# Kernel tuning notes

Hardware: AMD Instinct MI355X
Metric: run time of the kernel (lower is better)

Reference implementation:

```python
import jax, jax.numpy as jnp
import numpy as np

B, L, E, H = 4, 4096, 1024, 16
HD = E // H
I = 4096  # intermediate_size = 4*E
RMS_EPS = 1e-6
ATTN_EPS = 1e-6
GATE_INIT = 0.1  # 0.1 + 0.05*layer_idx, layer_idx=0


def rmsnorm(x, w, eps=RMS_EPS):
    xf = x.astype(jnp.float32)
    var = jnp.mean(xf * xf, axis=-1, keepdims=True)
    return w * (xf * jax.lax.rsqrt(var + eps)).astype(x.dtype)


def rotate_half(x):
    d = x.shape[-1] // 2
    return jnp.concatenate([-x[..., d:], x[..., :d]], axis=-1)


def setup_inputs() -> dict:
    key = jax.random.key(0)
    ks = jax.random.split(key, 16)
    h = jax.random.normal(ks[0], (B, L, E), jnp.float32)
    c = jax.random.normal(ks[1], (B, E), jnp.float32)
    # standard RoPE tables, shape (L, HD)
    pos = jnp.arange(L, dtype=jnp.float32)
    inv = 1.0 / (10000.0 ** (jnp.arange(0, HD, 2, dtype=jnp.float32) / HD))
    fr = pos[:, None] * inv[None, :]
    emb = jnp.concatenate([fr, fr], axis=-1)
    cos, sin = jnp.cos(emb), jnp.sin(emb)
    s = 0.02
    Wq = jax.random.normal(ks[2], (E, E), jnp.float32) * s
    Wk = jax.random.normal(ks[3], (E, E), jnp.float32) * s
    Wv = jax.random.normal(ks[4], (E, E), jnp.float32) * s
    Wo = jax.random.normal(ks[5], (E, E), jnp.float32) * s
    Wg = jax.random.normal(ks[6], (I, E), jnp.float32) * s
    Wu = jax.random.normal(ks[7], (I, E), jnp.float32) * s
    Wd = jax.random.normal(ks[8], (E, I), jnp.float32) * s
    w_norm1 = jnp.ones((E,), jnp.float32)
    w_norm2 = jnp.ones((E,), jnp.float32)
    Wada = jax.random.normal(ks[9], (6 * E, E), jnp.float32) * 0.01
    bada = np.zeros((6 * E,), np.float32)
    bada[2 * E:3 * E] = GATE_INIT  # gate_msa
    bada[5 * E:6 * E] = GATE_INIT  # gate_mlp
    bada = jnp.asarray(bada)
    return {"h": h, "c": c, "cos": cos, "sin": sin, "Wq": Wq, "Wk": Wk,
            "Wv": Wv, "Wo": Wo, "Wg": Wg, "Wu": Wu, "Wd": Wd,
            "w_norm1": w_norm1, "w_norm2": w_norm2, "Wada": Wada, "bada": bada}


def reference(h, c, cos, sin, Wq, Wk, Wv, Wo, Wg, Wu, Wd, w_norm1, w_norm2, Wada, bada):
    # adaLN modulation: (B, 6E) -> six (B,1,E) chunks
    mod = c @ Wada.T + bada
    sh1, sc1, g1, sh2, sc2, g2 = [m[:, None, :] for m in jnp.split(mod, 6, axis=-1)]

    # --- attention branch ---
    x = rmsnorm(h, w_norm1) * (1.0 + sc1) + sh1  # modulate
    q = jax.nn.silu(x @ Wq.T).reshape(B, L, H, HD).transpose(0, 2, 1, 3)  # (B,H,L,hd)
    k = jax.nn.silu(x @ Wk.T).reshape(B, L, H, HD).transpose(0, 2, 1, 3)
    v = (x @ Wv.T).reshape(B, L, H, HD).transpose(0, 2, 1, 3)
    cs = cos[None, None]  # (1,1,L,hd)
    sn = sin[None, None]
    q = q * cs + rotate_half(q) * sn
    k = k * cs + rotate_half(k) * sn
    # cosFormer sin/cos feature map; m = max(src,tgt) = L
    idx = (np.pi / 2) * jnp.arange(1, L + 1, dtype=jnp.float32) / L  # (L,)
    sw = jnp.sin(idx)[None, None, :, None]
    cw = jnp.cos(idx)[None, None, :, None]
    q_ = jnp.concatenate([q * sw, q * cw], axis=-1)  # (B,H,L,2hd)
    k_ = jnp.concatenate([k * sw, k * cw], axis=-1)
    # non-causal linear attention: K^T V first (O(L))
    kv = jnp.einsum('bhld,bhlm->bhdm', k_, v)             # (B,H,2hd,hd)
    z = 1.0 / jnp.maximum(jnp.einsum('bhld,bhd->bhl', q_, k_.sum(axis=2)), ATTN_EPS)
    attn = jnp.einsum('bhld,bhdm,bhl->bhlm', q_, kv, z)   # (B,H,L,hd)
    attn = attn.transpose(0, 2, 1, 3).reshape(B, L, E) @ Wo.T
    h = h + g1 * attn  # bias_dropout_add_scale, eval mode

    # --- MLP branch ---
    x = rmsnorm(h, w_norm2) * (1.0 + sc2) + sh2
    mlp = (jax.nn.silu(x @ Wg.T) * (x @ Wu.T)) @ Wd.T
    return h + g2 * mlp
```

## Files before the change

### kernel.cpp

```cpp
#include <hip/hip_runtime.h>
#include <hip/hip_bf16.h>

#define BB 4
#define LL 4096
#define EE 1024
#define HH 16
#define II 4096
#define MM (BB*LL)

using f32x4 = __attribute__((ext_vector_type(4))) float;
using s16x8 = __attribute__((ext_vector_type(8))) short;
using u32x4 = __attribute__((ext_vector_type(4))) unsigned int;

__device__ __forceinline__ unsigned short f2bf(float f) {
  union { float f; unsigned u; } x; x.f = f;
  unsigned r = x.u + 0x7fffu + ((x.u >> 16) & 1u);
  return (unsigned short)(r >> 16);
}
__device__ __forceinline__ float bf2f(unsigned short s) {
  union { unsigned u; float f; } x; x.u = ((unsigned)s) << 16;
  return x.f;
}
__device__ __forceinline__ float silu_f(float x) { return x / (1.0f + expf(-x)); }

__device__ __forceinline__ void gll16(const void* g, void* l) {
  __builtin_amdgcn_global_load_lds(
      (const __attribute__((address_space(1))) unsigned int*)g,
      (__attribute__((address_space(3))) unsigned int*)l, 16, 0, 0);
}

__global__ __launch_bounds__(256) void k_mod(const float* __restrict__ c,
    const float* __restrict__ Wada, const float* __restrict__ bada,
    float* __restrict__ mod) {
  __shared__ float cs[EE];
  int b = blockIdx.y;
  int n = blockIdx.x * 256 + threadIdx.x;
  for (int i = threadIdx.x; i < EE; i += 256) cs[i] = c[b*EE + i];
  __syncthreads();
  const float4* wp = (const float4*)(Wada + (size_t)n * EE);
  float acc = 0.f;
  for (int k = 0; k < EE/4; k++) {
    float4 t = wp[k];
    acc += t.x*cs[4*k] + t.y*cs[4*k+1] + t.z*cs[4*k+2] + t.w*cs[4*k+3];
  }
  mod[(size_t)b*6*EE + n] = acc + bada[n];
}

__global__ __launch_bounds__(256) void k_coef(const float* __restrict__ mod,
    const float* __restrict__ w1, const float* __restrict__ w2,
    float* __restrict__ cf1, float* __restrict__ cf2) {
  int k = blockIdx.x * 256 + threadIdx.x;
  int b = blockIdx.y;
  const float* mb = mod + (size_t)b*6*EE;
  cf1[(size_t)b*2048 + k]        = w1[k] * (1.0f + mb[EE + k]);
  cf1[(size_t)b*2048 + 1024 + k] = mb[k];
  cf2[(size_t)b*2048 + k]        = w2[k] * (1.0f + mb[4*EE + k]);
  cf2[(size_t)b*2048 + 1024 + k] = mb[3*EE + k];
}

__global__ __launch_bounds__(256) void k_rsig(const float* __restrict__ in,
    float* __restrict__ rsig) {
  int row = blockIdx.x;
  int t = threadIdx.x;
  float4 v = ((const float4*)(in + (size_t)row * EE))[t];
  float ss = v.x*v.x + v.y*v.y + v.z*v.z + v.w*v.w;
  #pragma unroll
  for (int o = 32; o > 0; o >>= 1) ss += __shfl_down(ss, o, 64);
  __shared__ float red[4];
  if ((t & 63) == 0) red[t >> 6] = ss;
  __syncthreads();
  float tot = red[0] + red[1] + red[2] + red[3];
  if (t == 0) rsig[row] = 1.0f / sqrtf(tot * (1.0f/1024.0f) + 1e-6f);
}

__global__ __launch_bounds__(256) void k_f2b(const float* __restrict__ s,
    unsigned short* __restrict__ d, int n4) {
  int i = blockIdx.x * 256 + threadIdx.x;
  if (i >= n4) return;
  float4 v = ((const float4*)s)[i];
  ushort4 u; u.x = f2bf(v.x); u.y = f2bf(v.y); u.z = f2bf(v.z); u.w = f2bf(v.w);
  ((ushort4*)d)[i] = u;
}

__global__ __launch_bounds__(256) void k_split1(const float* __restrict__ h,
    const float* __restrict__ rsig, const float* __restrict__ cf,
    unsigned short* __restrict__ xh, unsigned short* __restrict__ xl) {
  int row = blockIdx.x;
  int t = threadIdx.x;
  int b = row >> 12;
  float rs = rsig[row];
  const float* cfb = cf + (size_t)b*2048;
  float4 v  = ((const float4*)(h + (size_t)row*EE))[t];
  float4 c1 = ((const float4*)cfb)[t];
  float4 c0 = ((const float4*)(cfb + 1024))[t];
  float x0 = fmaf(v.x*rs, c1.x, c0.x);
  float x1 = fmaf(v.y*rs, c1.y, c0.y);
  float x2 = fmaf(v.z*rs, c1.z, c0.z);
  float x3 = fmaf(v.w*rs, c1.w, c0.w);
  ushort4 uh, ul;
  uh.x = f2bf(x0); ul.x = f2bf(x0 - bf2f(uh.x));
  uh.y = f2bf(x1); ul.y = f2bf(x1 - bf2f(uh.y));
  uh.z = f2bf(x2); ul.z = f2bf(x2 - bf2f(uh.z));
  uh.w = f2bf(x3); ul.w = f2bf(x3 - bf2f(uh.w));
  ((ushort4*)(xh + (size_t)row*EE))[t] = uh;
  ((ushort4*)(xl + (size_t)row*EE))[t] = ul;
}

__global__ __launch_bounds__(256) void k_split2(const float* __restrict__ in,
    const float* __restrict__ rsig, const float* __restrict__ cf,
    unsigned short* __restrict__ xb) {
  int row = blockIdx.x;
  int t = threadIdx.x;
  int b = row >> 12;
  float rs = rsig[row];
  const float* cfb = cf + (size_t)b*2048;
  float4 v  = ((const float4*)(in + (size_t)row*EE))[t];
  float4 c1 = ((const float4*)cfb)[t];
  float4 c0 = ((const float4*)(cfb + 1024))[t];
  ushort4 u;
  u.x = f2bf(fmaf(v.x*rs, c1.x, c0.x));
  u.y = f2bf(fmaf(v.y*rs, c1.y, c0.y));
  u.z = f2bf(fmaf(v.z*rs, c1.z, c0.z));
  u.w = f2bf(fmaf(v.w*rs, c1.w, c0.w));
  ((ushort4*)(xb + (size_t)row*EE))[t] = u;
}

__global__ __launch_bounds__(256) void k_sgemmK(
    const float* __restrict__ Ah, const float* __restrict__ W,
    const float* __restrict__ rsig, const float* __restrict__ cf,
    const float* __restrict__ cosT, const float* __restrict__ sinT,
    float* __restrict__ outq) {
  __shared__ float As[8][128];
  __shared__ float Bs[8][128];
  __shared__ float c1s[1024];
  __shared__ float c0s[1024];
  int t = threadIdx.x;
  int tx = t & 15, ty = t >> 4;
  int bm = blockIdx.x, bn = blockIdx.y;
  int srow = t >> 1, sk = (t & 1) * 4;
  int bidx = bm >> 5;
  for (int i = t; i < 1024; i += 256) {
    c1s[i] = cf[(size_t)bidx*2048 + i];
    c0s[i] = cf[(size_t)bidx*2048 + 1024 + i];
  }
  int arow = bm*128 + srow;
  float rsA = rsig[arow];
  const float* ap = Ah + (size_t)arow*EE + sk;
  const float* bp = W + (size_t)(bn*128 + srow)*EE + sk;
  float acc[8][8];
  #pragma unroll
  for (int i = 0; i < 8; i++)
    #pragma unroll
    for (int j = 0; j < 8; j++) acc[i][j] = 0.f;
  float4 pa = *(const float4*)ap;
  float4 pb = *(const float4*)bp;
  int c0 = (tx < 8) ? tx*4 : 64 + (tx - 8)*4;
  __syncthreads();
  for (int k0 = 0; k0 < EE; k0 += 8) {
    int kb = k0 + sk;
    As[sk+0][srow] = fmaf(pa.x*rsA, c1s[kb+0], c0s[kb+0]);
    As[sk+1][srow] = fmaf(pa.y*rsA, c1s[kb+1], c0s[kb+1]);
    As[sk+2][srow] = fmaf(pa.z*rsA, c1s[kb+2], c0s[kb+2]);
    As[sk+3][srow] = fmaf(pa.w*rsA, c1s[kb+3], c0s[kb+3]);
    Bs[sk+0][srow] = pb.x; Bs[sk+1][srow] = pb.y; Bs[sk+2][srow] = pb.z; Bs[sk+3][srow] = pb.w;
    __syncthreads();
    if (k0 + 8 < EE) {
      pa = *(const float4*)(ap + k0 + 8);
      pb = *(const float4*)(bp + k0 + 8);
    }
    #pragma unroll
    for (int k = 0; k < 8; k++) {
      float4 a0 = *(const float4*)&As[k][ty*8];
      float4 a1 = *(const float4*)&As[k][ty*8+4];
      float4 b0 = *(const float4*)&Bs[k][c0];
      float4 b1 = *(const float4*)&Bs[k][c0+32];
      float av[8] = {a0.x,a0.y,a0.z,a0.w,a1.x,a1.y,a1.z,a1.w};
      float bv[8]  = {b0.x,b0.y,b0.z,b0.w,b1.x,b1.y,b1.z,b1.w};
      #pragma unroll
      for (int i = 0; i < 8; i++)
        #pragma unroll
        for (int j = 0; j < 8; j++)
          acc[i][j] = fmaf(av[i], bv[j], acc[i][j]);
    }
    __syncthreads();
  }
  int head = bn*2 + (tx >= 8 ? 1 : 0);
  int d0 = (tx < 8) ? tx*4 : (tx - 8)*4;
  #pragma unroll
  for (int i = 0; i < 8; i++) {
    int m = bm*128 + ty*8 + i;
    int b = m >> 12, l = m & 4095;
    const float* cp = cosT + (size_t)l*64;
    const float* sp = sinT + (size_t)l*64;
    float4 cl  = *(const float4*)(cp + d0);
    float4 slv = *(const float4*)(sp + d0);
    float4 chv = *(const float4*)(cp + d0 + 32);
    float4 shv = *(const float4*)(sp + d0 + 32);
    float sA0 = silu_f(acc[i][0]), sA1 = silu_f(acc[i][1]), sA2 = silu_f(acc[i][2]), sA3 = silu_f(acc[i][3]);
    float sB0 = silu_f(acc[i][4]), sB1 = silu_f(acc[i][5]), sB2 = silu_f(acc[i][6]), sB3 = silu_f(acc[i][7]);
    float q00 = sA0*cl.x - sB0*slv.x;
    float q01 = sA1*cl.y - sB1*slv.y;
    float q02 = sA2*cl.z - sB2*slv.z;
    float q03 = sA3*cl.w - sB3*slv.w;
    float q10 = sB0*chv.x + sA0*shv.x;
    float q11 = sB1*chv.y + sA1*shv.y;
    float q12 = sB2*chv.z + sA2*shv.z;
    float q13 = sB3*chv.w + sA3*shv.w;
    float* op = outq + ((size_t)(b*HH + head)*LL + l)*64;
    *(float4*)(op + d0)      = make_float4(q00, q01, q02, q03);
    *(float4*)(op + d0 + 32) = make_float4(q10, q11, q12, q13);
  }
}

__global__ __launch_bounds__(256) void k_qk(
    const unsigned short* __restrict__ xh, const unsigned short* __restrict__ xl,
    const float* __restrict__ W,
    const float* __restrict__ cosT, const float* __restrict__ sinT,
    float* __restrict__ outq) {
  __shared__ unsigned short Ah[128*32];
  __shared__ unsigned short Al[128*32];
  __shared__ unsigned short Bh[64*40];
  __shared__ unsigned short Bl[64*40];
  int t = threadIdx.x, w = t >> 6, lane = t & 63;
  int bm = blockIdx.x, bn = blockIdx.y;
  int wm = (w & 1) * 64;
  int wn = (w >> 1) * 16;
  int r16 = lane & 15, kg = lane >> 4;
  int rin = lane >> 2, slot = lane & 3;
  int ar0 = w*32 + rin, ar1 = ar0 + 16;
  const unsigned short* ahg0 = xh + (size_t)(bm*128 + ar0)*EE + (size_t)((((ar0>>1)&3) ^ slot) * 8);
  const unsigned short* ahg1 = xh + (size_t)(bm*128 + ar1)*EE + (size_t)((((ar1>>1)&3) ^ slot) * 8);
  const unsigned short* alg0 = xl + (size_t)(bm*128 + ar0)*EE + (size_t)((((ar0>>1)&3) ^ slot) * 8);
  const unsigned short* alg1 = xl + (size_t)(bm*128 + ar1)*EE + (size_t)((((ar1>>1)&3) ^ slot) * 8);
  unsigned short* ahl0 = &Ah[(w*32 + 0) * 32];
  unsigned short* ahl1 = &Ah[(w*32 + 16) * 32];
  unsigned short* all0 = &Al[(w*32 + 0) * 32];
  unsigned short* all1 = &Al[(w*32 + 16) * 32];
  int srow = t >> 2, koff = (t & 3) * 8;
  const float* bp = W + (size_t)(bn*64 + srow)*EE + koff;
  float4 pb0 = *(const float4*)(bp + 0);
  float4 pb1 = *(const float4*)(bp + 4);
  f32x4 acc[4][2];
  #pragma unroll
  for (int i = 0; i < 4; i++) { acc[i][0] = (f32x4){0,0,0,0}; acc[i][1] = (f32x4){0,0,0,0}; }

  for (int k0 = 0; k0 < EE; k0 += 32) {
    gll16(ahg0 + k0, ahl0);
    gll16(ahg1 + k0, ahl1);
    gll16(alg0 + k0, all0);
    gll16(alg1 + k0, all1);
    {
      unsigned short h0 = f2bf(pb0.x), h1 = f2bf(pb0.y), h2 = f2bf(pb0.z), h3 = f2bf(pb0.w);
      unsigned short h4 = f2bf(pb1.x), h5 = f2bf(pb1.y), h6 = f2bf(pb1.z), h7 = f2bf(pb1.w);
      unsigned short l0 = f2bf(pb0.x - bf2f(h0)), l1 = f2bf(pb0.y - bf2f(h1));
      unsigned short l2 = f2bf(pb0.z - bf2f(h2)), l3 = f2bf(pb0.w - bf2f(h3));
      unsigned short l4 = f2bf(pb1.x - bf2f(h4)), l5 = f2bf(pb1.y - bf2f(h5));
      unsigned short l6 = f2bf(pb1.z - bf2f(h6)), l7 = f2bf(pb1.w - bf2f(h7));
      u32x4 uh, ul;
      uh[0] = ((unsigned)h1<<16)|h0; uh[1] = ((unsigned)h3<<16)|h2;
      uh[2] = ((unsigned)h5<<16)|h4; uh[3] = ((unsigned)h7<<16)|h6;
      ul[0] = ((unsigned)l1<<16)|l0; ul[1] = ((unsigned)l3<<16)|l2;
      ul[2] = ((unsigned)l5<<16)|l4; ul[3] = ((unsigned)l7<<16)|l6;
      *(u32x4*)&Bh[srow*40 + koff] = uh;
      *(u32x4*)&Bl[srow*40 + koff] = ul;
    }
    __syncthreads();
    if (k0 + 32 < EE) {
      pb0 = *(const float4*)(bp + k0 + 32);
      pb1 = *(const float4*)(bp + k0 + 36);
    }
    int brow0 = wn + r16, brow1 = wn + 32 + r16;
    s16x8 bh0 = *(const s16x8*)&Bh[brow0*40 + kg*8];
    s16x8 bl0 = *(const s16x8*)&Bl[brow0*40 + kg*8];
    s16x8 bh1 = *(const s16x8*)&Bh[brow1*40 + kg*8];
    s16x8 bl1 = *(const s16x8*)&Bl[brow1*40 + kg*8];
    #pragma unroll
    for (int i = 0; i < 4; i++) {
      int row = wm + i*16 + r16;
      int sw = ((((row>>1)&3) ^ kg) << 3);
      s16x8 ah = *(const s16x8*)&Ah[row*32 + sw];
      s16x8 al = *(const s16x8*)&Al[row*32 + sw];
      acc[i][0] = __builtin_amdgcn_mfma_f32_16x16x32_bf16(ah, bh0, acc[i][0], 0, 0, 0);
      acc[i][0] = __builtin_amdgcn_mfma_f32_16x16x32_bf16(ah, bl0, acc[i][0], 0, 0, 0);
      acc[i][0] = __builtin_amdgcn_mfma_f32_16x16x32_bf16(al, bh0, acc[i][0], 0, 0, 0);
      acc[i][1] = __builtin_amdgcn_mfma_f32_16x16x32_bf16(ah, bh1, acc[i][1], 0, 0, 0);
      acc[i][1] = __builtin_amdgcn_mfma_f32_16x16x32_bf16(ah, bl1, acc[i][1], 0, 0, 0);
      acc[i][1] = __builtin_amdgcn_mfma_f32_16x16x32_bf16(al, bh1, acc[i][1], 0, 0, 0);
    }
    __syncthreads();
  }
  int d = wn + r16;
  #pragma unroll
  for (int i = 0; i < 4; i++) {
    #pragma unroll
    for (int r = 0; r < 4; r++) {
      int mm = bm*128 + wm + i*16 + kg*4 + r;
      int b = mm >> 12, l = mm & 4095;
      const float* cp = cosT + (size_t)l*64;
      const float* sp = sinT + (size_t)l*64;
      float sl = silu_f(acc[i][0][r]);
      float sh = silu_f(acc[i][1][r]);
      float qlo = sl*cp[d]      - sh*sp[d];
      float qhi = sh*cp[d + 32] + sl*sp[d + 32];
      float* op = outq + (((size_t)(b*HH + bn))*LL + l)*64;
      op[d]      = qlo;
      op[d + 32] = qhi;
    }
  }
}

template<int EPI, int KLEN, int SA, int SB>
__global__ __launch_bounds__(256) void k_gemm2(
    const unsigned short* __restrict__ Ab,
    const unsigned short* __restrict__ Bw,
    int kbB, int bnoff,
    const float* __restrict__ res, const float* __restrict__ mod,
    unsigned short* __restrict__ outb, float* __restrict__ outf) {
  __shared__ unsigned short As[128 * 32];
  __shared__ unsigned short Bs[128 * 32];
  int t = threadIdx.x, w = t >> 6, lane = t & 63;
  int bm = blockIdx.x, bn = blockIdx.y;
  int wm = (w >> 1) * 64, wn = (w & 1) * 64;
  int rin = lane >> 2, slot = lane & 3;
  int brow0 = w*32 + rin, brow1 = brow0 + 16;
  int swz0 = (((brow0>>1)&3) ^ slot) * 8;
  int swz1 = (((brow1>>1)&3) ^ slot) * 8;
  const unsigned short* ag0 = Ab + (size_t)(bm*128 + brow0)*SA + swz0;
  const unsigned short* ag1 = Ab + (size_t)(bm*128 + brow1)*SA + swz1;
  const unsigned short* bg0 = Bw + (size_t)(bnoff + bn*128 + brow0)*SB + kbB + swz0;
  const unsigned short* bg1 = Bw + (size_t)(bnoff + bn*128 + brow1)*SB + kbB + swz1;
  unsigned short* al0 = &As[(w*32 + 0) * 32];
  unsigned short* al1 = &As[(w*32 + 16) * 32];
  unsigned short* bl0 = &Bs[(w*32 + 0) * 32];
  unsigned short* bl1 = &Bs[(w*32 + 16) * 32];
  f32x4 acc[4][4];
  #pragma unroll
  for (int i = 0; i < 4; i++)
    #pragma unroll
    for (int j = 0; j < 4; j++) acc[i][j] = (f32x4){0.f, 0.f, 0.f, 0.f};
  int r16 = lane & 15, kg = lane >> 4;
  for (int k0 = 0; k0 < KLEN; k0 += 32) {
    gll16(ag0 + k0, al0);
    gll16(ag1 + k0, al1);
    gll16(bg0 + k0, bl0);
    gll16(bg1 + k0, bl1);
    __syncthreads();
    s16x8 af[4], bfr[4];
    #pragma unroll
    for (int i = 0; i < 4; i++) {
      int row = wm + i*16 + r16;
      af[i] = *(const s16x8*)&As[row*32 + ((((row>>1)&3) ^ kg) << 3)];
    }
    #pragma unroll
    for (int j = 0; j < 4; j++) {
      int row = wn + j*16 + r16;
      bfr[j] = *(const s16x8*)&Bs[row*32 + ((((row>>1)&3) ^ kg) << 3)];
    }
    #pragma unroll
    for (int i = 0; i < 4; i++)
      #pragma unroll
      for (int j = 0; j < 4; j++)
        acc[i][j] = __builtin_amdgcn_mfma_f32_16x16x32_bf16(af[i], bfr[j], acc[i][j], 0, 0, 0);
    __syncthreads();
  }
  #pragma unroll
  for (int i = 0; i < 4; i++) {
    #pragma unroll
    for (int j = 0; j < 4; j++) {
      int nn = bn*128 + wn + j*16 + r16;
      #pragma unroll
      for (int r = 0; r < 4; r++) {
        int mm = bm*128 + wm + i*16 + kg*4 + r;
        float v = acc[i][j][r];
        if constexpr (EPI == 0) {
          int b = mm >> 12, l = mm & 4095, hh = nn >> 6, dd = nn & 63;
          outb[(((size_t)(b*HH + hh))*LL + l)*64 + dd] = f2bf(v);
        } else if constexpr (EPI == 1) {
          int b = mm >> 12;
          size_t o = (size_t)mm*EE + nn;
          outf[o] = res[o] + mod[(size_t)b*6*EE + 2*EE + nn] * v;
        } else {
          int b = mm >> 12;
          size_t o = (size_t)mm*EE + nn;
          outf[o] = res[o] + mod[(size_t)b*6*EE + 5*EE + nn] * v;
        }
      }
    }
  }
}

__global__ __launch_bounds__(256) void k_gemmGU(
    const unsigned short* __restrict__ Ab,
    const unsigned short* __restrict__ Wg, const unsigned short* __restrict__ Wu,
    int bnoff, unsigned short* __restrict__ outP) {
  __shared__ unsigned short As[128 * 32];
  __shared__ unsigned short Bg[128 * 32];
  __shared__ unsigned short Bu[128 * 32];
  int t = threadIdx.x, w = t >> 6, lane = t & 63;
  int bm = blockIdx.x, bn = blockIdx.y;
  int wm = (w >> 1) * 64, wn = (w & 1) * 64;
  int rin = lane >> 2, slot = lane & 3;
  int brow0 = w*32 + rin, brow1 = brow0 + 16;
  int swz0 = (((brow0>>1)&3) ^ slot) * 8;
  int swz1 = (((brow1>>1)&3) ^ slot) * 8;
  const unsigned short* ag0 = Ab + (size_t)(bm*128 + brow0)*EE + swz0;
  const unsigned short* ag1 = Ab + (size_t)(bm*128 + brow1)*EE + swz1;
  size_t boff0 = (size_t)(bnoff + bn*128 + brow0)*EE + swz0;
  size_t boff1 = (size_t)(bnoff + bn*128 + brow1)*EE + swz1;
  const unsigned short* bg0 = Wg + boff0;
  const unsigned short* bg1 = Wg + boff1;
  const unsigned short* bu0 = Wu + boff0;
  const unsigned short* bu1 = Wu + boff1;
  unsigned short* al0  = &As[(w*32 + 0) * 32];
  unsigned short* al1  = &As[(w*32 + 16) * 32];
  unsigned short* blg0 = &Bg[(w*32 + 0) * 32];
  unsigned short* blg1 = &Bg[(w*32 + 16) * 32];
  unsigned short* blu0 = &Bu[(w*32 + 0) * 32];
  unsigned short* blu1 = &Bu[(w*32 + 16) * 32];
  f32x4 accg[4][4], accu[4][4];
  #pragma unroll
  for (int i = 0; i < 4; i++)
    #pragma unroll
    for (int j = 0; j < 4; j++) {
      accg[i][j] = (f32x4){0.f, 0.f, 0.f, 0.f};
      accu[i][j] = (f32x4){0.f, 0.f, 0.f, 0.f};
    }
  int r16 = lane & 15, kg = lane >> 4;
  for (int k0 = 0; k0 < EE; k0 += 32) {
    gll16(ag0 + k0, al0);
    gll16(ag1 + k0, al1);
    gll16(bg0 + k0, blg0);
    gll16(bg1 + k0, blg1);
    gll16(bu0 + k0, blu0);
    gll16(bu1 + k0, blu1);
    __syncthreads();
    s16x8 af[4], bgf[4], buf[4];
    #pragma unroll
    for (int i = 0; i < 4; i++) {
      int row = wm + i*16 + r16;
      af[i] = *(const s16x8*)&As[row*32 + ((((row>>1)&3) ^ kg) << 3)];
    }
    #pragma unroll
    for (int j = 0; j < 4; j++) {
      int row = wn + j*16 + r16;
      int sw = row*32 + ((((row>>1)&3) ^ kg) << 3);
      bgf[j] = *(const s16x8*)&Bg[sw];
      buf[j] = *(const s16x8*)&Bu[sw];
    }
    #pragma unroll
    for (int i = 0; i < 4; i++)
      #pragma unroll
      for (int j = 0; j < 4; j++) {
        accg[i][j] = __builtin_amdgcn_mfma_f32_16x16x32_bf16(af[i], bgf[j], accg[i][j], 0, 0, 0);
        accu[i][j] = __builtin_amdgcn_mfma_f32_16x16x32_bf16(af[i], buf[j], accu[i][j], 0, 0, 0);
      }
    __syncthreads();
  }
  #pragma unroll
  for (int i = 0; i < 4; i++) {
    #pragma unroll
    for (int j = 0; j < 4; j++) {
      int nn = bn*128 + wn + j*16 + r16;
      #pragma unroll
      for (int r = 0; r < 4; r++) {
        int mm = bm*128 + wm + i*16 + kg*4 + r;
        outP[(size_t)mm*2048 + nn] = f2bf(silu_f(accg[i][j][r]) * accu[i][j][r]);
      }
    }
  }
}

__global__ __launch_bounds__(256) void k_kvpart(const float* __restrict__ kr,
    const unsigned short* __restrict__ vtb, float* __restrict__ kvp) {
  int bi = blockIdx.x;
  int bh = bi >> 3, ch = bi & 7;
  const float* kp = kr + ((size_t)bh*LL + ch*512)*64;
  const unsigned short* vp = vtb + ((size_t)bh*LL + ch*512)*64;
  __shared__ float k8[8][64];
  __shared__ float v8[8][64];
  __shared__ float sw8[8], cw8[8];
  int t = threadIdx.x;
  int d = t >> 2, mq = (t & 3) * 16;
  float accS[16], accC[16];
  #pragma unroll
  for (int q = 0; q < 16; q++) { accS[q] = 0.f; accC[q] = 0.f; }
  float ksS = 0.f, ksC = 0.f;
  for (int l0 = 0; l0 < 512; l0 += 8) {
    __syncthreads();
    #pragma unroll
    for (int rep = 0; rep < 2; rep++) {
      int idx = rep*256 + t;
      k8[idx>>6][idx&63] = kp[(size_t)(l0 + (idx>>6))*64 + (idx&63)];
      v8[idx>>6][idx&63] = bf2f(vp[(size_t)(l0 + (idx>>6))*64 + (idx&63)]);
    }
    if (t < 8) {
      int gl = ch*512 + l0 + t;
      float idxv = 1.5707964f * (float)(gl + 1) * (1.0f/4096.0f);
      sw8[t] = sinf(idxv);
      cw8[t] = cosf(idxv);
    }
    __syncthreads();
    #pragma unroll
    for (int l = 0; l < 8; l++) {
      float kd = k8[l][d];
      float s = kd * sw8[l];
      float c = kd * cw8[l];
      ksS += s; ksC += c;
      const float4* vv = (const float4*)&v8[l][mq];
      #pragma unroll
      for (int q = 0; q < 4; q++) {
        float4 x = vv[q];
        accS[4*q+0] = fmaf(s, x.x, accS[4*q+0]);
        accS[4*q+1] = fmaf(s, x.y, accS[4*q+1]);
        accS[4*q+2] = fmaf(s, x.z, accS[4*q+2]);
        accS[4*q+3] = fmaf(s, x.w, accS[4*q+3]);
        accC[4*q+0] = fmaf(c, x.x, accC[4*q+0]);
        accC[4*q+1] = fmaf(c, x.y, accC[4*q+1]);
        accC[4*q+2] = fmaf(c, x.z, accC[4*q+2]);
        accC[4*q+3] = fmaf(c, x.w, accC[4*q+3]);
      }
    }
  }
  float* op = kvp + (size_t)bi * 8320;
  #pragma unroll
  for (int q = 0; q < 16; q++) {
    op[d*64 + mq + q]        = accS[q];
    op[4096 + d*64 + mq + q] = accC[q];
  }
  if (mq == 0) { op[8192 + d] = ksS; op[8256 + d] = ksC; }
}

__global__ __launch_bounds__(256) void k_kvred(const float* __restrict__ kvp,
    float* __restrict__ kvb, int* __restrict__ cnt) {
  int bh = blockIdx.x;
  if (bh == 0 && threadIdx.x == 0) *cnt = 0;
  for (int i = threadIdx.x; i < 8320; i += 256) {
    float s = 0.f;
    #pragma unroll
    for (int c = 0; c < 8; c++) s += kvp[((size_t)bh*8 + c)*8320 + i];
    kvb[(size_t)bh*8320 + i] = s;
  }
}

__global__ __launch_bounds__(256) void k_z(const float* __restrict__ qr,
    const float* __restrict__ kvb, float* __restrict__ zb,
    int* __restrict__ list, int* __restrict__ cnt) {
  int bh = blockIdx.x >> 6, lc = blockIdx.x & 63;
  __shared__ float ksS_s[64], ksC_s[64];
  int t = threadIdx.x;
  if (t < 64) ksS_s[t] = kvb[(size_t)bh*8320 + 8192 + t];
  else if (t < 128) ksC_s[t-64] = kvb[(size_t)bh*8320 + 8256 + (t-64)];
  __syncthreads();
  int l = lc*64 + (t >> 2), part = t & 3;
  const float4* qp = (const float4*)(qr + ((size_t)bh*LL + l)*64 + part*16);
  float A = 0.f, Bv = 0.f;
  #pragma unroll
  for (int q = 0; q < 4; q++) {
    float4 x = qp[q];
    int kb = part*16 + 4*q;
    A  += x.x*ksS_s[kb] + x.y*ksS_s[kb+1] + x.z*ksS_s[kb+2] + x.w*ksS_s[kb+3];
    Bv += x.x*ksC_s[kb] + x.y*ksC_s[kb+1] + x.z*ksC_s[kb+2] + x.w*ksC_s[kb+3];
  }
  A  += __shfl_xor(A, 1, 64);  A  += __shfl_xor(A, 2, 64);
  Bv += __shfl_xor(Bv, 1, 64); Bv += __shfl_xor(Bv, 2, 64);
  if (part == 0) {
    float idxv = 1.5707964f * (float)(l + 1) * (1.0f/4096.0f);
    float denom = sinf(idxv)*A + cosf(idxv)*Bv;
    int gid = bh*LL + l;
    zb[gid] = 1.0f / fmaxf(denom, 1e-6f);
    if (fabsf(denom) < 0.05f) {
      int idx = atomicAdd(cnt, 1);
      if (idx < 8000) list[idx] = gid;
    }
  }
}

__global__ __launch_bounds__(256) void k_zfix(const float* __restrict__ h,
    const float* __restrict__ rsig, const float* __restrict__ cf,
    const float* __restrict__ Wq,
    const float* __restrict__ cosT, const float* __restrict__ sinT,
    const float* __restrict__ kvb, const int* __restrict__ list,
    const int* __restrict__ cnt, float* __restrict__ zb) {
  __shared__ float xs[1024];
  __shared__ double qd[64];
  __shared__ double sq[64];
  int n = *cnt;
  if (n > 8000) n = 8000;
  int t = threadIdx.x;
  for (int i = blockIdx.x; i < n; i += gridDim.x) {
    int gid = list[i];
    int bh = gid >> 12, l = gid & 4095;
    int b = bh >> 4, hh = bh & 15;
    int row = b*4096 + l;
    float rs = rsig[row];
    const float* cfb = cf + (size_t)b*2048;
    for (int k = t; k < 1024; k += 256)
      xs[k] = fmaf(h[(size_t)row*1024 + k]*rs, cfb[k], cfb[1024 + k]);
    __syncthreads();
    int j = t >> 2, s = t & 3;
    const float* wrow = Wq + (size_t)(hh*64 + j)*1024 + s*256;
    double acc = 0.0;
    for (int k = 0; k < 256; k++)
      acc += (double)wrow[k] * (double)xs[s*256 + k];
    acc += __shfl_xor(acc, 1, 64);
    acc += __shfl_xor(acc, 2, 64);
    if (s == 0) qd[j] = acc;
    __syncthreads();
    if (t < 64) {
      double qv = qd[t];
      sq[t] = qv / (1.0 + exp(-qv));
    }
    __syncthreads();
    if (t == 0) {
      const float* cp = cosT + (size_t)l*64;
      const float* sp = sinT + (size_t)l*64;
      const float* ksS = kvb + (size_t)bh*8320 + 8192;
      const float* ksC = kvb + (size_t)bh*8320 + 8256;
      double dS = 0.0, dC = 0.0;
      for (int d = 0; d < 64; d++) {
        double rot = (d < 32) ? -sq[d + 32] : sq[d - 32];
        double qe = sq[d]*(double)cp[d] + rot*(double)sp[d];
        dS += qe * (double)ksS[d];
        dC += qe * (double)ksC[d];
      }
      double idxv = 1.5707963267948966 * (double)(l + 1) / 4096.0;
      float denom = (float)(sin(idxv)*dS + cos(idxv)*dC);
      zb[gid] = 1.0f / fmaxf(denom, 1e-6f);
    }
    __syncthreads();
  }
}

__global__ __launch_bounds__(256) void k_attn(const float* __restrict__ qr,
    const float* __restrict__ kvb, const float* __restrict__ zb,
    unsigned short* __restrict__ attnb) {
  int bh = blockIdx.x >> 4, lc = blockIdx.x & 15;
  int t = threadIdx.x, w = t >> 6, lane = t & 63;
  const float* kvp_ = kvb + (size_t)bh*8320;
  float kvS[64], kvC[64];
  #pragma unroll
  for (int d = 0; d < 64; d++) kvS[d] = kvp_[d*64 + lane];
  #pragma unroll
  for (int d = 0; d < 64; d++) kvC[d] = kvp_[4096 + d*64 + lane];
  int b = bh >> 4, hh = bh & 15;
  int lbase = lc*256 + w*64;
  for (int li = 0; li < 64; li++) {
    int l = lbase + li;
    const float* qp = qr + ((size_t)bh*LL + l)*64;
    float qv = qp[lane];
    float z = zb[(size_t)bh*LL + l];
    float a0 = 0.f, a1 = 0.f, a2 = 0.f, a3 = 0.f;
    float b0 = 0.f, b1 = 0.f, b2 = 0.f, b3 = 0.f;
    #pragma unroll
    for (int d = 0; d < 64; d += 4) {
      float q0 = __uint_as_float(__builtin_amdgcn_readlane(__float_as_uint(qv), d+0));
      float q1 = __uint_as_float(__builtin_amdgcn_readlane(__float_as_uint(qv), d+1));
      float q2 = __uint_as_float(__builtin_amdgcn_readlane(__float_as_uint(qv), d+2));
      float q3 = __uint_as_float(__builtin_amdgcn_readlane(__float_as_uint(qv), d+3));
      a0 = fmaf(q0, kvS[d+0], a0);
      a1 = fmaf(q1, kvS[d+1], a1);
      a2 = fmaf(q2, kvS[d+2], a2);
      a3 = fmaf(q3, kvS[d+3], a3);
      b0 = fmaf(q0, kvC[d+0], b0);
      b1 = fmaf(q1, kvC[d+1], b1);
      b2 = fmaf(q2, kvC[d+2], b2);
      b3 = fmaf(q3, kvC[d+3], b3);
    }
    float A = (a0 + a1) + (a2 + a3);
    float Bv = (b0 + b1) + (b2 + b3);
    float idxv = 1.5707964f * (float)(l + 1) * (1.0f/4096.0f);
    float num = sinf(idxv)*A + cosf(idxv)*Bv;
    attnb[(((size_t)b*LL + l)*HH + hh)*64 + lane] = f2bf(num * z);
  }
}

extern "C" void kernel_launch(void* const* d_in, const int* in_sizes, int n_in,
                              void* d_out, int out_size, void* d_ws, size_t ws_size,
                              hipStream_t stream) {
  const float* h    = (const float*)d_in[0];
  const float* c    = (const float*)d_in[1];
  const float* cosT = (const float*)d_in[2];
  const float* sinT = (const float*)d_in[3];
  const float* Wq   = (const float*)d_in[4];
  const float* Wk   = (const float*)d_in[5];
  const float* Wv   = (const float*)d_in[6];
  const float* Wo   = (const float*)d_in[7];
  const float* Wg   = (const float*)d_in[8];
  const float* Wu   = (const float*)d_in[9];
  const float* Wd   = (const float*)d_in[10];
  const float* w1   = (const float*)d_in[11];
  const float* w2   = (const float*)d_in[12];
  const float* Wada = (const float*)d_in[13];
  const float* bada = (const float*)d_in[14];
  float* out = (float*)d_out;

  constexpr size_t BIG_SZ   = (size_t)MM * II * 2;
  constexpr size_t WS_NEEDED = BIG_SZ + 131072 + 32768*2 + 65536*2
      + 1048576 + 2129920 + 2097152*2 + 8388608*3;
  if (ws_size < WS_NEEDED) return;

  char* p = (char*)d_ws;
  char* big = p;                               p += BIG_SZ;
  float* mod = (float*)p;                      p += 131072;
  float* cf1 = (float*)p;                      p += 32768;
  float* cf2 = (float*)p;                      p += 32768;
  float* rsig1 = (float*)p;                    p += 65536;
  float* rsig2 = (float*)p;                    p += 65536;
  float* zb  = (float*)p;                      p += 1048576;
  float* kvb = (float*)p;                      p += 2129920;
  unsigned short* Wvb = (unsigned short*)p;    p += 2097152;
  unsigned short* Wob = (unsigned short*)p;    p += 2097152;
  unsigned short* Wgb = (unsigned short*)p;    p += 8388608;
  unsigned short* Wub = (unsigned short*)p;    p += 8388608;
  unsigned short* Wdb = (unsigned short*)p;    p += 8388608;
  int* zf_cnt  = (int*)((char*)mod + 98304);
  int* zf_list = zf_cnt + 64;
  unsigned short* xh   = (unsigned short*)big;
  unsigned short* xl   = (unsigned short*)(big + 33554432);
  unsigned short* vtb  = (unsigned short*)(big + 67108864);
  float* kvp           = (float*)(big + 100663296);
  float* qr            = (float*)(big + 67108864);
  unsigned short* attnb= (unsigned short*)big;
  unsigned short* x2b  = (unsigned short*)big;
  unsigned short* Pb   = (unsigned short*)(big + 33554432);
  float* kr            = (float*)d_out;

  k_mod<<<dim3(24, BB), 256, 0, stream>>>(c, Wada, bada, mod);
  k_coef<<<dim3(4, BB), 256, 0, stream>>>(mod, w1, w2, cf1, cf2);
  k_rsig<<<MM, 256, 0, stream>>>(h, rsig1);
  k_f2b<<<1024, 256, 0, stream>>>(Wv, Wvb, EE*EE/4);
  k_f2b<<<1024, 256, 0, stream>>>(Wo, Wob, EE*EE/4);
  k_f2b<<<4096, 256, 0, stream>>>(Wg, Wgb, II*EE/4);
  k_f2b<<<4096, 256, 0, stream>>>(Wu, Wub, II*EE/4);
  k_f2b<<<4096, 256, 0, stream>>>(Wd, Wdb, EE*II/4);
  k_split1<<<MM, 256, 0, stream>>>(h, rsig1, cf1, xh, xl);

  k_sgemmK<<<dim3(128, 8), 256, 0, stream>>>(h, Wk, rsig1, cf1, cosT, sinT, kr);
  k_gemm2<0, EE, EE, EE><<<dim3(128, 8), 256, 0, stream>>>(
      xh, Wvb, 0, 0, nullptr, nullptr, vtb, nullptr);
  k_kvpart<<<BB*HH*8, 256, 0, stream>>>(kr, vtb, kvp);
  k_kvred<<<BB*HH, 256, 0, stream>>>(kvp, kvb, zf_cnt);

  k_qk<<<dim3(128, 16), 256, 0, stream>>>(xh, xl, Wq, cosT, sinT, qr);
  k_z<<<BB*HH*(LL/64), 256, 0, stream>>>(qr, kvb, zb, zf_list, zf_cnt);
  k_zfix<<<120, 256, 0, stream>>>(h, rsig1, cf1, Wq, cosT, sinT, kvb,
                                  zf_list, zf_cnt, zb);
  k_attn<<<BB*HH*(LL/256), 256, 0, stream>>>(qr, kvb, zb, attnb);

  k_gemm2<1, EE, EE, EE><<<dim3(128, 8), 256, 0, stream>>>(
      attnb, Wob, 0, 0, h, mod, nullptr, out);

  k_rsig<<<MM, 256, 0, stream>>>(out, rsig2);
  k_split2<<<MM, 256, 0, stream>>>(out, rsig2, cf2, x2b);
  for (int half = 0; half < 2; half++) {
    k_gemmGU<<<dim3(128, 16), 256, 0, stream>>>(
        x2b, Wgb, Wub, half*2048, Pb);
    k_gemm2<4, 2048, 2048, II><<<dim3(128, 8), 256, 0, stream>>>(
        Pb, Wdb, half*2048, 0, out, mod, nullptr, out);
  }
}
```

Before: 1.995 ms.

## Co-schedule K and V projections in one kernel; split gate/up GEMM

The fp32 K projection and the bf16 MFMA V projection now run in one launch, with even and odd blocks taking different roles over a shared 16 KB LDS buffer, so the two independent GEMMs can overlap on the GPU. Separately, the fused gate/up GEMM is replaced by two generic GEMM launches: one writes silu(gate) as bf16 and the other reads it back and multiplies by up. The second change cuts per-block LDS and accumulator registers, which may raise occupancy, but it reads the A operand twice and adds a bf16 round-trip of the intermediate, which costs traffic and a little precision.

```diff
diff --git a/kernel.cpp b/kernel.cpp
--- a/kernel.cpp
+++ b/kernel.cpp
@@ -125,18 +125,17 @@
   ((ushort4*)(xb + (size_t)row*EE))[t] = u;
 }
 
-__global__ __launch_bounds__(256) void k_sgemmK(
+__device__ void role_sgemmK(char* smem, int bm, int bn,
     const float* __restrict__ Ah, const float* __restrict__ W,
     const float* __restrict__ rsig, const float* __restrict__ cf,
     const float* __restrict__ cosT, const float* __restrict__ sinT,
     float* __restrict__ outq) {
-  __shared__ float As[8][128];
-  __shared__ float Bs[8][128];
-  __shared__ float c1s[1024];
-  __shared__ float c0s[1024];
+  float (*As)[128] = (float(*)[128])(smem);
+  float (*Bs)[128] = (float(*)[128])(smem + 4096);
+  float* c1s = (float*)(smem + 8192);
+  float* c0s = (float*)(smem + 12288);
   int t = threadIdx.x;
   int tx = t & 15, ty = t >> 4;
-  int bm = blockIdx.x, bn = blockIdx.y;
   int srow = t >> 1, sk = (t & 1) * 4;
   int bidx = bm >> 5;
   for (int i = t; i < 1024; i += 256) {
@@ -209,6 +208,87 @@
     float* op = outq + ((size_t)(b*HH + head)*LL + l)*64;
     *(float4*)(op + d0)      = make_float4(q00, q01, q02, q03);
     *(float4*)(op + d0 + 32) = make_float4(q10, q11, q12, q13);
+  }
+}
+
+__device__ void role_v(char* smem, int bm, int bn,
+    const unsigned short* __restrict__ Ab, const unsigned short* __restrict__ Bw,
+    unsigned short* __restrict__ outb) {
+  unsigned short* As = (unsigned short*)smem;
+  unsigned short* Bs = (unsigned short*)(smem + 8192);
+  int t = threadIdx.x, w = t >> 6, lane = t & 63;
+  int wm = (w >> 1) * 64, wn = (w & 1) * 64;
+  int rin = lane >> 2, slot = lane & 3;
+  int brow0 = w*32 + rin, brow1 = brow0 + 16;
+  int swz0 = (((brow0>>1)&3) ^ slot) * 8;
+  int swz1 = (((brow1>>1)&3) ^ slot) * 8;
+  const unsigned short* ag0 = Ab + (size_t)(bm*128 + brow0)*EE + swz0;
+  const unsigned short* ag1 = Ab + (size_t)(bm*128 + brow1)*EE + swz1;
+  const unsigned short* bg0 = Bw + (size_t)(bn*128 + brow0)*EE + swz0;
+  const unsigned short* bg1 = Bw + (size_t)(bn*128 + brow1)*EE + swz1;
+  unsigned short* al0 = &As[(w*32 + 0) * 32];
+  unsigned short* al1 = &As[(w*32 + 16) * 32];
+  unsigned short* bl0 = &Bs[(w*32 + 0) * 32];
+  unsigned short* bl1 = &Bs[(w*32 + 16) * 32];
+  f32x4 acc[4][4];
+  #pragma unroll
+  for (int i = 0; i < 4; i++)
+    #pragma unroll
+    for (int j = 0; j < 4; j++) acc[i][j] = (f32x4){0.f, 0.f, 0.f, 0.f};
+  int r16 = lane & 15, kg = lane >> 4;
+  for (int k0 = 0; k0 < EE; k0 += 32) {
+    gll16(ag0 + k0, al0);
+    gll16(ag1 + k0, al1);
+    gll16(bg0 + k0, bl0);
+    gll16(bg1 + k0, bl1);
+    __syncthreads();
+    s16x8 af[4], bfr[4];
+    #pragma unroll
+    for (int i = 0; i < 4; i++) {
+      int row = wm + i*16 + r16;
+      af[i] = *(const s16x8*)&As[row*32 + ((((row>>1)&3) ^ kg) << 3)];
+    }
+    #pragma unroll
+    for (int j = 0; j < 4; j++) {
+      int row = wn + j*16 + r16;
+      bfr[j] = *(const s16x8*)&Bs[row*32 + ((((row>>1)&3) ^ kg) << 3)];
+    }
+    #pragma unroll
+    for (int i = 0; i < 4; i++)
+      #pragma unroll
+      for (int j = 0; j < 4; j++)
+        acc[i][j] = __builtin_amdgcn_mfma_f32_16x16x32_bf16(af[i], bfr[j], acc[i][j], 0, 0, 0);
+    __syncthreads();
+  }
+  #pragma unroll
+  for (int i = 0; i < 4; i++) {
+    #pragma unroll
+    for (int j = 0; j < 4; j++) {
+      int nn = bn*128 + wn + j*16 + r16;
+      #pragma unroll
+      for (int r = 0; r < 4; r++) {
+        int mm = bm*128 + wm + i*16 + kg*4 + r;
+        int b = mm >> 12, l = mm & 4095, hh = nn >> 6, dd = nn & 63;
+        outb[(((size_t)(b*HH + hh))*LL + l)*64 + dd] = f2bf(acc[i][j][r]);
+      }
+    }
+  }
+}
+
+__global__ __launch_bounds__(256) void k_megaKV(
+    const float* __restrict__ h, const float* __restrict__ Wk,
+    const float* __restrict__ rsig, const float* __restrict__ cf,
+    const float* __restrict__ cosT, const float* __restrict__ sinT,
+    float* __restrict__ kr,
+    const unsigned short* __restrict__ xh,
+    const unsigned short* __restrict__ Wvb, unsigned short* __restrict__ vtb) {
+  __shared__ __align__(16) char smem[16384];
+  int bid = blockIdx.x;
+  int idx = bid >> 1;
+  if ((bid & 1) == 0) {
+    role_sgemmK(smem, idx & 127, idx >> 7, h, Wk, rsig, cf, cosT, sinT, kr);
+  } else {
+    role_v(smem, idx & 127, idx >> 7, xh, Wvb, vtb);
   }
 }
 
@@ -379,92 +459,16 @@
           int b = mm >> 12;
           size_t o = (size_t)mm*EE + nn;
           outf[o] = res[o] + mod[(size_t)b*6*EE + 2*EE + nn] * v;
+        } else if constexpr (EPI == 2) {
+          outb[(size_t)mm*2048 + nn] = f2bf(silu_f(v));
+        } else if constexpr (EPI == 3) {
+          size_t o = (size_t)mm*2048 + nn;
+          outb[o] = f2bf(bf2f(outb[o]) * v);
         } else {
           int b = mm >> 12;
           size_t o = (size_t)mm*EE + nn;
           outf[o] = res[o] + mod[(size_t)b*6*EE + 5*EE + nn] * v;
         }
-      }
-    }
-  }
-}
-
-__global__ __launch_bounds__(256) void k_gemmGU(
-    const unsigned short* __restrict__ Ab,
-    const unsigned short* __restrict__ Wg, const unsigned short* __restrict__ Wu,
-    int bnoff, unsigned short* __restrict__ outP) {
-  __shared__ unsigned short As[128 * 32];
-  __shared__ unsigned short Bg[128 * 32];
-  __shared__ unsigned short Bu[128 * 32];
-  int t = threadIdx.x, w = t >> 6, lane = t & 63;
-  int bm = blockIdx.x, bn = blockIdx.y;
-  int wm = (w >> 1) * 64, wn = (w & 1) * 64;
-  int rin = lane >> 2, slot = lane & 3;
-  int brow0 = w*32 + rin, brow1 = brow0 + 16;
-  int swz0 = (((brow0>>1)&3) ^ slot) * 8;
-  int swz1 = (((brow1>>1)&3) ^ slot) * 8;
-  const unsigned short* ag0 = Ab + (size_t)(bm*128 + brow0)*EE + swz0;
-  const unsigned short* ag1 = Ab + (size_t)(bm*128 + brow1)*EE + swz1;
-  size_t boff0 = (size_t)(bnoff + bn*128 + brow0)*EE + swz0;
-  size_t boff1 = (size_t)(bnoff + bn*128 + brow1)*EE + swz1;
-  const unsigned short* bg0 = Wg + boff0;
-  const unsigned short* bg1 = Wg + boff1;
-  const unsigned short* bu0 = Wu + boff0;
-  const unsigned short* bu1 = Wu + boff1;
-  unsigned short* al0  = &As[(w*32 + 0) * 32];
-  unsigned short* al1  = &As[(w*32 + 16) * 32];
-  unsigned short* blg0 = &Bg[(w*32 + 0) * 32];
-  unsigned short* blg1 = &Bg[(w*32 + 16) * 32];
-  unsigned short* blu0 = &Bu[(w*32 + 0) * 32];
-  unsigned short* blu1 = &Bu[(w*32 + 16) * 32];
-  f32x4 accg[4][4], accu[4][4];
-  #pragma unroll
-  for (int i = 0; i < 4; i++)
-    #pragma unroll
-    for (int j = 0; j < 4; j++) {
-      accg[i][j] = (f32x4){0.f, 0.f, 0.f, 0.f};
-      accu[i][j] = (f32x4){0.f, 0.f, 0.f, 0.f};
-    }
-  int r16 = lane & 15, kg = lane >> 4;
-  for (int k0 = 0; k0 < EE; k0 += 32) {
-    gll16(ag0 + k0, al0);
-    gll16(ag1 + k0, al1);
-    gll16(bg0 + k0, blg0);
-    gll16(bg1 + k0, blg1);
-    gll16(bu0 + k0, blu0);
-    gll16(bu1 + k0, blu1);
-    __syncthreads();
-    s16x8 af[4], bgf[4], buf[4];
-    #pragma unroll
-    for (int i = 0; i < 4; i++) {
-      int row = wm + i*16 + r16;
-      af[i] = *(const s16x8*)&As[row*32 + ((((row>>1)&3) ^ kg) << 3)];
-    }
-    #pragma unroll
-    for (int j = 0; j < 4; j++) {
-      int row = wn + j*16 + r16;
-      int sw = row*32 + ((((row>>1)&3) ^ kg) << 3);
-      bgf[j] = *(const s16x8*)&Bg[sw];
-      buf[j] = *(const s16x8*)&Bu[sw];
-    }
-    #pragma unroll
-    for (int i = 0; i < 4; i++)
-      #pragma unroll
-      for (int j = 0; j < 4; j++) {
-        accg[i][j] = __builtin_amdgcn_mfma_f32_16x16x32_bf16(af[i], bgf[j], accg[i][j], 0, 0, 0);
-        accu[i][j] = __builtin_amdgcn_mfma_f32_16x16x32_bf16(af[i], buf[j], accu[i][j], 0, 0, 0);
-      }
-    __syncthreads();
-  }
-  #pragma unroll
-  for (int i = 0; i < 4; i++) {
-    #pragma unroll
-    for (int j = 0; j < 4; j++) {
-      int nn = bn*128 + wn + j*16 + r16;
-      #pragma unroll
-      for (int r = 0; r < 4; r++) {
-        int mm = bm*128 + wm + i*16 + kg*4 + r;
-        outP[(size_t)mm*2048 + nn] = f2bf(silu_f(accg[i][j][r]) * accu[i][j][r]);
       }
     }
   }
@@ -735,9 +739,9 @@
   k_f2b<<<4096, 256, 0, stream>>>(Wd, Wdb, EE*II/4);
   k_split1<<<MM, 256, 0, stream>>>(h, rsig1, cf1, xh, xl);
 
-  k_sgemmK<<<dim3(128, 8), 256, 0, stream>>>(h, Wk, rsig1, cf1, cosT, sinT, kr);
-  k_gemm2<0, EE, EE, EE><<<dim3(128, 8), 256, 0, stream>>>(
-      xh, Wvb, 0, 0, nullptr, nullptr, vtb, nullptr);
+  k_megaKV<<<2048, 256, 0, stream>>>(h, Wk, rsig1, cf1, cosT, sinT, kr,
+                                     xh, Wvb, vtb);
+
   k_kvpart<<<BB*HH*8, 256, 0, stream>>>(kr, vtb, kvp);
   k_kvred<<<BB*HH, 256, 0, stream>>>(kvp, kvb, zf_cnt);
 
@@ -753,8 +757,10 @@
   k_rsig<<<MM, 256, 0, stream>>>(out, rsig2);
   k_split2<<<MM, 256, 0, stream>>>(out, rsig2, cf2, x2b);
   for (int half = 0; half < 2; half++) {
-    k_gemmGU<<<dim3(128, 16), 256, 0, stream>>>(
-        x2b, Wgb, Wub, half*2048, Pb);
+    k_gemm2<2, EE, EE, EE><<<dim3(128, 16), 256, 0, stream>>>(
+        x2b, Wgb, 0, half*2048, nullptr, nullptr, Pb, nullptr);
+    k_gemm2<3, EE, EE, EE><<<dim3(128, 16), 256, 0, stream>>>(
+        x2b, Wub, 0, half*2048, nullptr, nullptr, Pb, nullptr);
     k_gemm2<4, 2048, 2048, II><<<dim3(128, 8), 256, 0, stream>>>(
         Pb, Wdb, half*2048, 0, out, mod, nullptr, out);
   }
```

Result: no change. 1.991 ms (-0.2%).
